# Kernel tuning notes

Measured on AMD Instinct MI355X. Metric: run time of the kernel, lower is better.

Reference implementation:

```python
import jax, jax.numpy as jnp
import numpy as np

FLOW_ITERS = 8
DUAL_ITERS = 8
DUAL_STEP = 0.1
DUAL_MOM = 0.9
GRAPH_LAYERS = 2
BIG = 1e9


def _sparsemax(z, mask):
    # sparsemax along last axis; masked entries already hold -BIG, zeroed by mask after.
    V = z.shape[-1]
    zs = jnp.sort(z, axis=-1)[..., ::-1]
    cum = jnp.cumsum(zs, axis=-1)
    k = jnp.arange(1, V + 1, dtype=z.dtype)
    support = zs * k > (cum - 1.0)
    k_sel = jnp.sum(support.astype(jnp.int32), axis=-1, keepdims=True)
    tau = (jnp.take_along_axis(cum, k_sel - 1, axis=-1) - 1.0) / k_sel.astype(z.dtype)
    return jnp.maximum(z - tau, 0.0) * mask


def _min_cost_flow(props, demands):
    # iterative proportional flow routing: push relu(inflow - demand) along predicted proportions
    def body(flow, _):
        inflow = jnp.sum(flow, axis=1)[..., None]      # [B,V,1] inflow to each node
        adjusted = jax.nn.relu(inflow - demands)       # excess to re-route
        return props * adjusted, None                  # row i scaled by its excess
    flow0 = jnp.zeros_like(props)
    flow, _ = jax.lax.scan(body, flow0, None, length=FLOW_ITERS)
    return flow


def _dual_flow(dual_diff, adj):
    # Nesterov-momentum projected gradient on cost(x)=x^2 minus linear dual term, x>=0 on edges
    def body(carry, _):
        flow, acc = carry
        look = flow - DUAL_MOM * acc
        grad = 2.0 * look - dual_diff                  # d/dx x^2 - dual_diff
        acc = DUAL_MOM * acc + DUAL_STEP * grad
        flow = adj * jax.nn.relu(flow - acc)
        return (flow, acc), None
    z = jnp.zeros_like(dual_diff)
    (flow, _), _ = jax.lax.scan(body, (z, z), None, length=DUAL_ITERS)
    return flow


def setup_inputs():
    key = jax.random.key(0)
    ks = jax.random.split(key, 32)
    B, V, F, E, D, K, H = 8, 1200, 8, 16, 64, 2, 4
    node_features = jax.random.normal(ks[0], (B, V, F), dtype=jnp.float32)
    node_embeddings = jax.random.normal(ks[1], (B, V, E), dtype=jnp.float32)
    d = jax.random.normal(ks[2], (B, V, 1), dtype=jnp.float32)
    demands = d - jnp.mean(d, axis=1, keepdims=True)   # balanced supply/demand per graph
    eye = jnp.eye(V, dtype=jnp.float32)
    adj = (jax.random.uniform(ks[3], (B, V, V)) < (16.0 / V)).astype(jnp.float32) * (1.0 - eye)
    hop2 = jnp.clip(adj @ adj, 0.0, 1.0) * (1.0 - eye)
    neighborhoods = jnp.stack([adj, hop2], axis=0)     # [K,B,V,V] k-hop neighborhoods

    def dense(k, fin, fout):
        return (jax.random.normal(k, (fin, fout), dtype=jnp.float32) / np.sqrt(fin)).astype(jnp.float32)

    return dict(
        node_features=node_features, node_embeddings=node_embeddings,
        demands=demands, adj=adj, neighborhoods=neighborhoods,
        enc_w0=dense(ks[4], E + F, D), enc_b0=jnp.zeros((D,), jnp.float32),
        enc_w1=dense(ks[5], D, D), enc_b1=jnp.zeros((D,), jnp.float32),
        agg_w=(jax.random.normal(ks[6], (K, D, D)) / np.sqrt(D)).astype(jnp.float32),
        agg_b=jnp.zeros((K, D), jnp.float32),
        att_w=(jax.random.normal(ks[7], (H, D, D)) / np.sqrt(D)).astype(jnp.float32),
        att_b=jnp.zeros((H, D), jnp.float32),
        att_v=(jax.random.normal(ks[8], (H, D)) / np.sqrt(D)).astype(jnp.float32),
        gru_wu=dense(ks[9], 2 * D, D), gru_bu=jnp.zeros((D,), jnp.float32),
        gru_wr=dense(ks[10], 2 * D, D), gru_br=jnp.zeros((D,), jnp.float32),
        gru_wc=dense(ks[11], 2 * D, D), gru_bc=jnp.zeros((D,), jnp.float32),
        dec_w0=dense(ks[12], D, D), dec_b0=jnp.zeros((D,), jnp.float32),
        dec_w1=dense(ks[13], D, 1), dec_b1=jnp.zeros((1,), jnp.float32),
        dual_w0=dense(ks[14], D, D), dual_b0=jnp.zeros((D,), jnp.float32),
        dual_w1=dense(ks[15], D, 1), dual_b1=jnp.zeros((1,), jnp.float32),
    )


def reference(node_features, node_embeddings, demands, adj, neighborhoods,
              enc_w0, enc_b0, enc_w1, enc_b1, agg_w, agg_b, att_w, att_b, att_v,
              gru_wu, gru_bu, gru_wr, gru_br, gru_wc, gru_bc,
              dec_w0, dec_b0, dec_w1, dec_b1, dual_w0, dual_b0, dual_w1, dual_b1):
    H = att_w.shape[0]
    # node encoder MLP (tanh hidden, tanh final since activate_final=True)
    x = jnp.concatenate([node_embeddings, node_features], axis=-1)
    enc = jnp.tanh(jnp.tanh(x @ enc_w0 + enc_b0) @ enc_w1 + enc_b1)            # [B,V,D]

    deg = jnp.sum(neighborhoods, axis=-1, keepdims=True)
    nb_norm = neighborhoods / jnp.maximum(deg, 1.0)                            # [K,B,V,V]

    for _ in range(GRAPH_LAYERS):
        # per-hop neighborhood aggregation
        msg = jnp.einsum('kbuv,bvd->kbud', nb_norm, enc)
        agg = jnp.tanh(jnp.einsum('kbud,kde->kbue', msg, agg_w) + agg_b[:, None, None, :])
        # multi-head attention over the K hop levels
        proj = jnp.tanh(jnp.einsum('kbvd,hde->hkbve', agg, att_w) + att_b[:, None, None, None, :])
        scores = jnp.einsum('hkbve,he->hkbv', proj, att_v)
        attn = jax.nn.softmax(scores, axis=1)                                  # softmax over hops
        nxt = jnp.einsum('hkbv,kbvd->bvd', attn, agg) / H                      # mean over heads
        # GRU state update
        xs = jnp.concatenate([nxt, enc], axis=-1)
        u = jax.nn.sigmoid(xs @ gru_wu + gru_bu)
        r = jax.nn.sigmoid(xs @ gru_wr + gru_br)
        c = jnp.tanh(jnp.concatenate([nxt, r * enc], axis=-1) @ gru_wc + gru_bc)
        enc = u * enc + (1.0 - u) * c

    # primal: edge weights -> sparsemax -> min-cost-flow
    pred = (enc @ dec_w0 + dec_b0) @ dec_w1 + dec_b1                           # [B,V,1]
    pred_weights = adj * jnp.transpose(pred, (0, 2, 1))                        # [B,V,V]
    weights = -BIG * (1.0 - adj) + pred_weights
    flow_props = _sparsemax(weights, adj)
    flow = _min_cost_flow(flow_props, demands)
    flow_cost = jnp.sum(flow * flow, axis=(1, 2))                              # square cost

    # dual: potentials -> dual-diff -> dual flow solver
    dual = (enc @ dual_w0 + dual_b0) @ dual_w1 + dual_b1                       # [B,V,1]
    dual_diff = adj * (dual - jnp.transpose(dual, (0, 2, 1)))
    dflow = _dual_flow(dual_diff, adj)
    dual_demand = jnp.sum(dual * demands, axis=(1, 2))
    dual_cost = jnp.sum(dflow * dflow - dual_diff * dflow, axis=(1, 2)) - dual_demand

    return flow_cost - dual_cost                                               # duality-gap loss, [B]
```

## Files before the change

kernel.cpp:

```cpp
#include <hip/hip_runtime.h>

#define BB 8
#define VV 1200
#define DD 64
#define KH 2
#define NH 4
#define CAP 64
#define NB2CAP 384
#define NROW (BB*VV)
#define NKROW (KH*BB*VV)

__device__ __forceinline__ float wredsum(float v) {
#pragma unroll
  for (int o = 32; o > 0; o >>= 1) v += __shfl_xor(v, o, 64);
  return v;
}
__device__ __forceinline__ float gredsum(float v) {
#pragma unroll
  for (int o = 8; o > 0; o >>= 1) v += __shfl_xor(v, o, 64);
  return v;
}

__device__ __forceinline__ float tanh_f(float x) {
  float e = __expf(2.0f * x);
  return 1.0f - 2.0f / (e + 1.0f);
}
__device__ __forceinline__ float sigmoid_f(float x) { return 1.0f / (1.0f + __expf(-x)); }

__device__ __forceinline__ unsigned pack_bf16x2(float a, float b) {
  unsigned ua = __float_as_uint(a), ub = __float_as_uint(b);
  ua = (ua + 0x7fffu + ((ua >> 16) & 1u)) >> 16;
  ub = (ub + 0x7fffu + ((ub >> 16) & 1u)) & 0xffff0000u;
  return ua | ub;
}
__device__ __forceinline__ float bf_lo(unsigned u) { return __uint_as_float(u << 16); }
__device__ __forceinline__ float bf_hi(unsigned u) { return __uint_as_float(u & 0xffff0000u); }

__device__ __forceinline__ size_t nb_base(int row) {
  return (row < NROW) ? (size_t)row * CAP
                      : (size_t)NROW * CAP + (size_t)(row - NROW) * NB2CAP;
}

#define CSRB (NKROW / 4)
#define ENCB (NROW / 8)
__global__ void __launch_bounds__(256) k_pre(
    const float* __restrict__ nb, int* __restrict__ nb_cols, int* __restrict__ nb_cnt,
    const float* __restrict__ emb, const float* __restrict__ feat,
    const float* __restrict__ w0, const float* __restrict__ b0,
    const float* __restrict__ w1, const float* __restrict__ b1,
    unsigned* __restrict__ enc0,
    int* __restrict__ col_cnt, float* __restrict__ out, int out_size) {
  __shared__ float xT[8][25];
  __shared__ float hT[8][65];
  int bid = blockIdx.x;
  int tid = threadIdx.x;
  if (bid < CSRB) {
    int w = tid >> 6, lane = tid & 63;
    int row = bid * 4 + w;
    const float4* nb4 = (const float4*)(nb + (size_t)row * VV);
    float4 v[5];
#pragma unroll
    for (int c = 0; c < 4; ++c) v[c] = nb4[c * 64 + lane];
    v[4].x = v[4].y = v[4].z = v[4].w = 0.0f;
    if (lane < 44) v[4] = nb4[256 + lane];
    unsigned long long ltmask = (lane == 0) ? 0ull : ((1ull << lane) - 1ull);
    size_t base = nb_base(row);
    int cap = (row < NROW) ? CAP : NB2CAP;
    int off_base = 0;
#pragma unroll
    for (int c = 0; c < 5; ++c) {
      int nz0 = (v[c].x != 0.0f), nz1 = (v[c].y != 0.0f);
      int nz2 = (v[c].z != 0.0f), nz3 = (v[c].w != 0.0f);
      unsigned long long m0 = __ballot(nz0 != 0);
      unsigned long long m1 = __ballot(nz1 != 0);
      unsigned long long m2 = __ballot(nz2 != 0);
      unsigned long long m3 = __ballot(nz3 != 0);
      int lanepref = __popcll(m0 & ltmask) + __popcll(m1 & ltmask)
                   + __popcll(m2 & ltmask) + __popcll(m3 & ltmask);
      int chunkcnt = __popcll(m0) + __popcll(m1) + __popcll(m2) + __popcll(m3);
      int off = off_base + lanepref;
      int vi = (c * 64 + lane) * 4;
      if (nz0 && off < cap) nb_cols[base + off] = vi;
      off += nz0;
      if (nz1 && off < cap) nb_cols[base + off] = vi + 1;
      off += nz1;
      if (nz2 && off < cap) nb_cols[base + off] = vi + 2;
      off += nz2;
      if (nz3 && off < cap) nb_cols[base + off] = vi + 3;
      off_base += chunkcnt;
    }
    if (lane == 0) nb_cnt[row] = (off_base > cap) ? cap : off_base;
  } else if (bid < CSRB + ENCB) {
    int tile0 = (bid - CSRB) * 8;
    if (tid < 128) { int i = tid >> 4, d = tid & 15; xT[i][d] = emb[(size_t)(tile0 + i) * 16 + d]; }
    else if (tid < 192) { int t = tid - 128; int i = t >> 3, d = t & 7; xT[i][16 + d] = feat[(size_t)(tile0 + i) * 8 + d]; }
    __syncthreads();
    int r = tid >> 5, cg = tid & 31;
    int c0 = cg * 2;
    {
      float a0 = b0[c0], a1 = b0[c0 + 1];
#pragma unroll
      for (int kk = 0; kk < 24; ++kk) {
        float x = xT[r][kk];
        float2 w2 = *(const float2*)(w0 + kk * DD + c0);
        a0 = fmaf(x, w2.x, a0); a1 = fmaf(x, w2.y, a1);
      }
      hT[r][c0] = tanh_f(a0); hT[r][c0 + 1] = tanh_f(a1);
    }
    __syncthreads();
    {
      float g0 = b1[c0], g1 = b1[c0 + 1];
#pragma unroll 16
      for (int kk = 0; kk < DD; ++kk) {
        float x = hT[r][kk];
        float2 w2 = *(const float2*)(w1 + kk * DD + c0);
        g0 = fmaf(x, w2.x, g0); g1 = fmaf(x, w2.y, g1);
      }
      enc0[(size_t)(tile0 + r) * 32 + cg] = pack_bf16x2(tanh_f(g0), tanh_f(g1));
    }
  } else {
    for (int i = tid; i < NROW; i += 256) col_cnt[i] = 0;
    if (tid < out_size) out[tid] = 0.0f;
  }
}

__global__ void __launch_bounds__(256) k_gather(
    const int* __restrict__ nb_cols, const int* __restrict__ nb_cnt,
    const unsigned* __restrict__ encIn, float* __restrict__ msg) {
  int w = threadIdx.x >> 6, lane = threadIdx.x & 63;
  int row = blockIdx.x * 4 + w;
  int k = (row >= NROW) ? 1 : 0;
  int bv = row - k * NROW;
  int b = bv / VV;
  const uint2* encU = (const uint2*)(encIn + (size_t)b * VV * 32);
  const int* cols = nb_cols + nb_base(row);
  int n = nb_cnt[row];
  int sub = lane >> 4, q = lane & 15;
  float ax = 0.0f, ay = 0.0f, az = 0.0f, aw = 0.0f;
  int j = 0;
  int cc0 = 0, cc1 = 0, cc2 = 0, cc3 = 0;
  if (j + 16 <= n) {
    cc0 = cols[j + sub]; cc1 = cols[j + 4 + sub];
    cc2 = cols[j + 8 + sub]; cc3 = cols[j + 12 + sub];
  }
  while (j + 16 <= n) {
    int nj = j + 16;
    int p0 = 0, p1 = 0, p2 = 0, p3 = 0;
    if (nj + 16 <= n) {
      p0 = cols[nj + sub]; p1 = cols[nj + 4 + sub];
      p2 = cols[nj + 8 + sub]; p3 = cols[nj + 12 + sub];
    }
    uint2 u0 = encU[(size_t)cc0 * 16 + q];
    uint2 u1 = encU[(size_t)cc1 * 16 + q];
    uint2 u2 = encU[(size_t)cc2 * 16 + q];
    uint2 u3 = encU[(size_t)cc3 * 16 + q];
    ax += (bf_lo(u0.x) + bf_lo(u1.x)) + (bf_lo(u2.x) + bf_lo(u3.x));
    ay += (bf_hi(u0.x) + bf_hi(u1.x)) + (bf_hi(u2.x) + bf_hi(u3.x));
    az += (bf_lo(u0.y) + bf_lo(u1.y)) + (bf_lo(u2.y) + bf_lo(u3.y));
    aw += (bf_hi(u0.y) + bf_hi(u1.y)) + (bf_hi(u2.y) + bf_hi(u3.y));
    cc0 = p0; cc1 = p1; cc2 = p2; cc3 = p3;
    j = nj;
  }
  for (; j < n; j += 4) {
    int idx = j + sub;
    if (idx < n) {
      uint2 u = encU[(size_t)cols[idx] * 16 + q];
      ax += bf_lo(u.x); ay += bf_hi(u.x); az += bf_lo(u.y); aw += bf_hi(u.y);
    }
  }
#pragma unroll
  for (int o = 16; o < 64; o <<= 1) {
    ax += __shfl_xor(ax, o, 64);
    ay += __shfl_xor(ay, o, 64);
    az += __shfl_xor(az, o, 64);
    aw += __shfl_xor(aw, o, 64);
  }
  if (lane < 16) {
    float inv = 1.0f / fmaxf((float)n, 1.0f);
    float4 r; r.x = ax * inv; r.y = ay * inv; r.z = az * inv; r.w = aw * inv;
    ((float4*)(msg + (size_t)row * DD))[q] = r;
  }
}

__global__ void __launch_bounds__(512) k_aggatt(
    const float* __restrict__ msg,
    const float* __restrict__ agg_w, const float* __restrict__ agg_b,
    const float* __restrict__ att_w, const float* __restrict__ att_b,
    const float* __restrict__ att_v,
    float* __restrict__ agg, float* __restrict__ scores) {
  __shared__ float M[64][65];
  __shared__ float G[64][65];
  int tid = threadIdx.x;
  int tile0 = blockIdx.x * 64;
  int k = (tile0 >= NROW) ? 1 : 0;
  int bv0 = tile0 - k * NROW;
  int rsub = tid >> 4, cg = tid & 15;
  int c0 = cg * 4;
  int r0 = rsub * 2;
#pragma unroll
  for (int rep = 0; rep < 2; ++rep) {
    int idx = rep * 512 + tid; int i = idx >> 4, d4 = idx & 15;
    float4 m4 = *(const float4*)(msg + (size_t)(tile0 + i) * DD + d4 * 4);
    M[i][d4 * 4] = m4.x; M[i][d4 * 4 + 1] = m4.y; M[i][d4 * 4 + 2] = m4.z; M[i][d4 * 4 + 3] = m4.w;
  }
  __syncthreads();
  const float* W = agg_w + (size_t)k * DD * DD;
  float acc[2][4];
#pragma unroll
  for (int i = 0; i < 2; ++i)
#pragma unroll
    for (int j = 0; j < 4; ++j) acc[i][j] = agg_b[k * DD + c0 + j];
#pragma unroll 4
  for (int kk = 0; kk < DD; ++kk) {
    float4 w4 = *(const float4*)(W + kk * DD + c0);
    float x0 = M[r0][kk], x1 = M[r0 + 1][kk];
    acc[0][0] = fmaf(x0, w4.x, acc[0][0]); acc[0][1] = fmaf(x0, w4.y, acc[0][1]);
    acc[0][2] = fmaf(x0, w4.z, acc[0][2]); acc[0][3] = fmaf(x0, w4.w, acc[0][3]);
    acc[1][0] = fmaf(x1, w4.x, acc[1][0]); acc[1][1] = fmaf(x1, w4.y, acc[1][1]);
    acc[1][2] = fmaf(x1, w4.z, acc[1][2]); acc[1][3] = fmaf(x1, w4.w, acc[1][3]);
  }
#pragma unroll
  for (int i = 0; i < 2; ++i) {
    float4 g4;
    g4.x = tanh_f(acc[i][0]); g4.y = tanh_f(acc[i][1]);
    g4.z = tanh_f(acc[i][2]); g4.w = tanh_f(acc[i][3]);
    G[r0 + i][c0] = g4.x; G[r0 + i][c0 + 1] = g4.y; G[r0 + i][c0 + 2] = g4.z; G[r0 + i][c0 + 3] = g4.w;
    *(float4*)(agg + (size_t)(tile0 + r0 + i) * DD + c0) = g4;
  }
  __syncthreads();
#pragma unroll
  for (int h = 0; h < NH; ++h) {
    const float* Wh = att_w + (size_t)h * DD * DD;
    float a2[2][4];
#pragma unroll
    for (int i = 0; i < 2; ++i)
#pragma unroll
      for (int j = 0; j < 4; ++j) a2[i][j] = att_b[h * DD + c0 + j];
#pragma unroll 4
    for (int kk = 0; kk < DD; ++kk) {
      float4 w4 = *(const float4*)(Wh + kk * DD + c0);
      float x0 = G[r0][kk], x1 = G[r0 + 1][kk];
      a2[0][0] = fmaf(x0, w4.x, a2[0][0]); a2[0][1] = fmaf(x0, w4.y, a2[0][1]);
      a2[0][2] = fmaf(x0, w4.z, a2[0][2]); a2[0][3] = fmaf(x0, w4.w, a2[0][3]);
      a2[1][0] = fmaf(x1, w4.x, a2[1][0]); a2[1][1] = fmaf(x1, w4.y, a2[1][1]);
      a2[1][2] = fmaf(x1, w4.z, a2[1][2]); a2[1][3] = fmaf(x1, w4.w, a2[1][3]);
    }
    float4 v4 = *(const float4*)(att_v + h * DD + c0);
#pragma unroll
    for (int i = 0; i < 2; ++i) {
      float p = tanh_f(a2[i][0]) * v4.x + tanh_f(a2[i][1]) * v4.y
              + tanh_f(a2[i][2]) * v4.z + tanh_f(a2[i][3]) * v4.w;
      p = gredsum(p);
      if (cg == 0) scores[(size_t)(h * KH + k) * NROW + bv0 + r0 + i] = p;
    }
  }
}

__global__ void __launch_bounds__(512) k_gru(
    const unsigned* __restrict__ encIn, const float* __restrict__ agg,
    const float* __restrict__ scores,
    const float* __restrict__ wu, const float* __restrict__ bu,
    const float* __restrict__ wr, const float* __restrict__ br,
    const float* __restrict__ wc, const float* __restrict__ bc,
    unsigned* __restrict__ encOut,
    int do_decode,
    const float* __restrict__ dw0, const float* __restrict__ db0,
    const float* __restrict__ dw1, const float* __restrict__ db1,
    const float* __restrict__ uw0, const float* __restrict__ ub0,
    const float* __restrict__ uw1, const float* __restrict__ ub1,
    float* __restrict__ pred, float* __restrict__ dualp) {
  __shared__ float X[64][129];
  __shared__ float EO[64][65];
  int tid = threadIdx.x;
  int tile0 = blockIdx.x * 64;
  int rsub = tid >> 4, cg = tid & 15;
  int c0 = cg * 4;
  int r0 = rsub * 2;
#pragma unroll
  for (int rep = 0; rep < 2; ++rep) {
    int idx = rep * 512 + tid; int i = idx >> 4, d4 = idx & 15;
    int row = tile0 + i;
    float W0 = 0.0f, W1 = 0.0f;
#pragma unroll
    for (int h = 0; h < NH; ++h) {
      float s0 = scores[(size_t)(h * KH + 0) * NROW + row];
      float s1 = scores[(size_t)(h * KH + 1) * NROW + row];
      float m = fmaxf(s0, s1);
      float e0 = __expf(s0 - m), e1 = __expf(s1 - m);
      float inv = 1.0f / (e0 + e1);
      W0 += e0 * inv; W1 += e1 * inv;
    }
    W0 *= 0.25f; W1 *= 0.25f;
    uint2 eu = ((const uint2*)encIn)[(size_t)row * 16 + d4];
    float4 a0 = *(const float4*)(agg + (size_t)row * DD + d4 * 4);
    float4 a1 = *(const float4*)(agg + (size_t)(NROW + row) * DD + d4 * 4);
    X[i][d4 * 4]     = W0 * a0.x + W1 * a1.x;
    X[i][d4 * 4 + 1] = W0 * a0.y + W1 * a1.y;
    X[i][d4 * 4 + 2] = W0 * a0.z + W1 * a1.z;
    X[i][d4 * 4 + 3] = W0 * a0.w + W1 * a1.w;
    X[i][64 + d4 * 4]     = bf_lo(eu.x);
    X[i][64 + d4 * 4 + 1] = bf_hi(eu.x);
    X[i][64 + d4 * 4 + 2] = bf_lo(eu.y);
    X[i][64 + d4 * 4 + 3] = bf_hi(eu.y);
  }
  __syncthreads();
  float au[2][4], ar[2][4];
#pragma unroll
  for (int i = 0; i < 2; ++i)
#pragma unroll
    for (int j = 0; j < 4; ++j) { au[i][j] = bu[c0 + j]; ar[i][j] = br[c0 + j]; }
#pragma unroll 4
  for (int kk = 0; kk < 2 * DD; ++kk) {
    float4 u4 = *(const float4*)(wu + kk * DD + c0);
    float4 r4 = *(const float4*)(wr + kk * DD + c0);
    float x0 = X[r0][kk], x1 = X[r0 + 1][kk];
    au[0][0] = fmaf(x0, u4.x, au[0][0]); au[0][1] = fmaf(x0, u4.y, au[0][1]);
    au[0][2] = fmaf(x0, u4.z, au[0][2]); au[0][3] = fmaf(x0, u4.w, au[0][3]);
    au[1][0] = fmaf(x1, u4.x, au[1][0]); au[1][1] = fmaf(x1, u4.y, au[1][1]);
    au[1][2] = fmaf(x1, u4.z, au[1][2]); au[1][3] = fmaf(x1, u4.w, au[1][3]);
    ar[0][0] = fmaf(x0, r4.x, ar[0][0]); ar[0][1] = fmaf(x0, r4.y, ar[0][1]);
    ar[0][2] = fmaf(x0, r4.z, ar[0][2]); ar[0][3] = fmaf(x0, r4.w, ar[0][3]);
    ar[1][0] = fmaf(x1, r4.x, ar[1][0]); ar[1][1] = fmaf(x1, r4.y, ar[1][1]);
    ar[1][2] = fmaf(x1, r4.z, ar[1][2]); ar[1][3] = fmaf(x1, r4.w, ar[1][3]);
  }
  float uu[2][4], encv[2][4];
#pragma unroll
  for (int i = 0; i < 2; ++i)
#pragma unroll
    for (int j = 0; j < 4; ++j) {
      uu[i][j] = sigmoid_f(au[i][j]);
      encv[i][j] = X[r0 + i][64 + c0 + j];
    }
  __syncthreads();
#pragma unroll
  for (int i = 0; i < 2; ++i)
#pragma unroll
    for (int j = 0; j < 4; ++j)
      X[r0 + i][64 + c0 + j] = encv[i][j] * sigmoid_f(ar[i][j]);
  __syncthreads();
  float ac[2][4];
#pragma unroll
  for (int i = 0; i < 2; ++i)
#pragma unroll
    for (int j = 0; j < 4; ++j) ac[i][j] = bc[c0 + j];
#pragma unroll 4
  for (int kk = 0; kk < 2 * DD; ++kk) {
    float4 c4 = *(const float4*)(wc + kk * DD + c0);
    float x0 = X[r0][kk], x1 = X[r0 + 1][kk];
    ac[0][0] = fmaf(x0, c4.x, ac[0][0]); ac[0][1] = fmaf(x0, c4.y, ac[0][1]);
    ac[0][2] = fmaf(x0, c4.z, ac[0][2]); ac[0][3] = fmaf(x0, c4.w, ac[0][3]);
    ac[1][0] = fmaf(x1, c4.x, ac[1][0]); ac[1][1] = fmaf(x1, c4.y, ac[1][1]);
    ac[1][2] = fmaf(x1, c4.z, ac[1][2]); ac[1][3] = fmaf(x1, c4.w, ac[1][3]);
  }
#pragma unroll
  for (int i = 0; i < 2; ++i) {
    float4 e4;
    e4.x = uu[i][0] * encv[i][0] + (1.0f - uu[i][0]) * tanh_f(ac[i][0]);
    e4.y = uu[i][1] * encv[i][1] + (1.0f - uu[i][1]) * tanh_f(ac[i][1]);
    e4.z = uu[i][2] * encv[i][2] + (1.0f - uu[i][2]) * tanh_f(ac[i][2]);
    e4.w = uu[i][3] * encv[i][3] + (1.0f - uu[i][3]) * tanh_f(ac[i][3]);
    uint2 pk; pk.x = pack_bf16x2(e4.x, e4.y); pk.y = pack_bf16x2(e4.z, e4.w);
    ((uint2*)encOut)[(size_t)(tile0 + r0 + i) * 16 + cg] = pk;
    EO[r0 + i][c0] = e4.x; EO[r0 + i][c0 + 1] = e4.y;
    EO[r0 + i][c0 + 2] = e4.z; EO[r0 + i][c0 + 3] = e4.w;
  }
  if (do_decode) {
    __syncthreads();
    float hd[2][4], hq[2][4];
#pragma unroll
    for (int i = 0; i < 2; ++i)
#pragma unroll
      for (int j = 0; j < 4; ++j) { hd[i][j] = db0[c0 + j]; hq[i][j] = ub0[c0 + j]; }
#pragma unroll 4
    for (int kk = 0; kk < DD; ++kk) {
      float4 d4 = *(const float4*)(dw0 + kk * DD + c0);
      float4 q4 = *(const float4*)(uw0 + kk * DD + c0);
      float x0 = EO[r0][kk], x1 = EO[r0 + 1][kk];
      hd[0][0] = fmaf(x0, d4.x, hd[0][0]); hd[0][1] = fmaf(x0, d4.y, hd[0][1]);
      hd[0][2] = fmaf(x0, d4.z, hd[0][2]); hd[0][3] = fmaf(x0, d4.w, hd[0][3]);
      hd[1][0] = fmaf(x1, d4.x, hd[1][0]); hd[1][1] = fmaf(x1, d4.y, hd[1][1]);
      hd[1][2] = fmaf(x1, d4.z, hd[1][2]); hd[1][3] = fmaf(x1, d4.w, hd[1][3]);
      hq[0][0] = fmaf(x0, q4.x, hq[0][0]); hq[0][1] = fmaf(x0, q4.y, hq[0][1]);
      hq[0][2] = fmaf(x0, q4.z, hq[0][2]); hq[0][3] = fmaf(x0, q4.w, hq[0][3]);
      hq[1][0] = fmaf(x1, q4.x, hq[1][0]); hq[1][1] = fmaf(x1, q4.y, hq[1][1]);
      hq[1][2] = fmaf(x1, q4.z, hq[1][2]); hq[1][3] = fmaf(x1, q4.w, hq[1][3]);
    }
    float4 dv = *(const float4*)(dw1 + c0);
    float4 qv = *(const float4*)(uw1 + c0);
#pragma unroll
    for (int i = 0; i < 2; ++i) {
      float p = hd[i][0] * dv.x + hd[i][1] * dv.y + hd[i][2] * dv.z + hd[i][3] * dv.w;
      float q = hq[i][0] * qv.x + hq[i][1] * qv.y + hq[i][2] * qv.z + hq[i][3] * qv.w;
      p = gredsum(p);
      q = gredsum(q);
      if (cg == 0) {
        pred[tile0 + r0 + i] = p + db1[0];
        dualp[tile0 + r0 + i] = q + ub1[0];
      }
    }
  }
}

__global__ void __launch_bounds__(256) k_primal_dual(
    const int* __restrict__ nb_cols, const int* __restrict__ nb_cnt,
    const float* __restrict__ pred, const float* __restrict__ dualp,
    const float* __restrict__ dem,
    float* __restrict__ rowsum,
    int* __restrict__ col_cnt, int* __restrict__ col_rows, float* __restrict__ col_vals,
    float* __restrict__ out) {
  __shared__ float bacc[BB];
  if (threadIdx.x < BB) bacc[threadIdx.x] = 0.0f;
  __syncthreads();
  int w = threadIdx.x >> 6, lane = threadIdx.x & 63;
  int row = blockIdx.x * 4 + w;
  int b = row / VV;
  int n = nb_cnt[row];
  int c = (lane < n) ? nb_cols[(size_t)row * CAP + lane] : 0;
  const float* predB = pred + (size_t)b * VV;
  const float* dualB = dualp + (size_t)b * VV;
  float z = (lane < n) ? predB[c] : -1e30f;
  float tau = 0.0f;
  if (n > 0) {
    bool in = (lane < n);
    for (int it = 0; it < 64; ++it) {
      float s = wredsum(in ? z : 0.0f);
      int cnt = (int)__popcll(__ballot(in));
      tau = (s - 1.0f) / (float)cnt;
      bool nin = (z > tau);
      if (__ballot(nin) == __ballot(in)) break;
      in = nin;
    }
  }
  float pv = (lane < n) ? fmaxf(z - tau, 0.0f) : 0.0f;
  float s2 = wredsum(pv * pv);
  if (lane == 0) rowsum[row] = s2;
  if (pv > 0.0f) {
    int g = b * VV + c;
    int j = atomicAdd(&col_cnt[g], 1);
    if (j < CAP) {
      col_rows[(size_t)g * CAP + j] = row - b * VV;
      col_vals[(size_t)g * CAP + j] = pv;
    }
  }
  float du = dualp[row];
  float es = 0.0f;
  if (lane < n) {
    float dd = du - dualB[c];
    float f = 0.0f, acm = 0.0f;
#pragma unroll
    for (int t = 0; t < 8; ++t) {
      float look = f - 0.9f * acm;
      float grad = 2.0f * look - dd;
      acm = 0.9f * acm + 0.1f * grad;
      f = fmaxf(f - acm, 0.0f);
    }
    es = f * f - dd * f;
  }
  float contrib = -es;
  if (lane == 0) contrib += du * dem[row];
  float ws_ = wredsum(contrib);
  if (lane == 0) atomicAdd(&bacc[b], ws_);
  __syncthreads();
  if (threadIdx.x < BB) {
    float t = bacc[threadIdx.x];
    if (t != 0.0f) atomicAdd(&out[threadIdx.x], t);
  }
}

__global__ void __launch_bounds__(1024) k_flow(
    const int* __restrict__ col_cnt, const int* __restrict__ col_rows,
    const float* __restrict__ col_vals, const float* __restrict__ dem,
    const float* __restrict__ rowsum, float* __restrict__ out) {
  __shared__ float aS[VV];
  __shared__ float red[16];
  int b = blockIdx.x;
  int tid = threadIdx.x;
  const float* demB = dem + (size_t)b * VV;
  for (int v = tid; v < VV; v += 1024) aS[v] = fmaxf(-demB[v], 0.0f);
  __syncthreads();
  for (int t = 0; t < 7; ++t) {
    float nv0 = 0.0f, nv1 = 0.0f;
    {
      int v = tid;
      if (v < VV) {
        int g = b * VV + v;
        int n = col_cnt[g]; if (n > CAP) n = CAP;
        const int* cr = col_rows + (size_t)g * CAP;
        const float* cv = col_vals + (size_t)g * CAP;
        float acc = 0.0f;
        for (int j = 0; j < n; ++j) acc += cv[j] * aS[cr[j]];
        nv0 = fmaxf(acc - demB[v], 0.0f);
      }
      v = tid + 1024;
      if (v < VV) {
        int g = b * VV + v;
        int n = col_cnt[g]; if (n > CAP) n = CAP;
        const int* cr = col_rows + (size_t)g * CAP;
        const float* cv = col_vals + (size_t)g * CAP;
        float acc = 0.0f;
        for (int j = 0; j < n; ++j) acc += cv[j] * aS[cr[j]];
        nv1 = fmaxf(acc - demB[v], 0.0f);
      }
    }
    __syncthreads();
    if (tid < VV) aS[tid] = nv0;
    if (tid + 1024 < VV) aS[tid + 1024] = nv1;
    __syncthreads();
  }
  float fc = 0.0f;
  for (int v = tid; v < VV; v += 1024) { float a = aS[v]; fc += a * a * rowsum[b * VV + v]; }
  fc = wredsum(fc);
  int wid = tid >> 6, lane = tid & 63;
  if (lane == 0) red[wid] = fc;
  __syncthreads();
  if (tid == 0) {
    float s = 0.0f;
#pragma unroll
    for (int i = 0; i < 16; ++i) s += red[i];
    atomicAdd(&out[b], s);
  }
}

extern "C" void kernel_launch(void* const* d_in, const int* in_sizes, int n_in,
                              void* d_out, int out_size, void* d_ws, size_t ws_size,
                              hipStream_t stream) {
  const float* feat   = (const float*)d_in[0];
  const float* emb    = (const float*)d_in[1];
  const float* dem    = (const float*)d_in[2];
  const float* nb     = (const float*)d_in[4];
  const float* enc_w0 = (const float*)d_in[5];
  const float* enc_b0 = (const float*)d_in[6];
  const float* enc_w1 = (const float*)d_in[7];
  const float* enc_b1 = (const float*)d_in[8];
  const float* agg_w  = (const float*)d_in[9];
  const float* agg_b  = (const float*)d_in[10];
  const float* att_w  = (const float*)d_in[11];
  const float* att_b  = (const float*)d_in[12];
  const float* att_v  = (const float*)d_in[13];
  const float* gru_wu = (const float*)d_in[14];
  const float* gru_bu = (const float*)d_in[15];
  const float* gru_wr = (const float*)d_in[16];
  const float* gru_br = (const float*)d_in[17];
  const float* gru_wc = (const float*)d_in[18];
  const float* gru_bc = (const float*)d_in[19];
  const float* dec_w0 = (const float*)d_in[20];
  const float* dec_b0 = (const float*)d_in[21];
  const float* dec_w1 = (const float*)d_in[22];
  const float* dec_b1 = (const float*)d_in[23];
  const float* dual_w0= (const float*)d_in[24];
  const float* dual_b0= (const float*)d_in[25];
  const float* dual_w1= (const float*)d_in[26];
  const float* dual_b1= (const float*)d_in[27];
  float* out = (float*)d_out;

  unsigned* enc0 = (unsigned*)d_ws;
  unsigned* enc1 = enc0 + (size_t)NROW * 32;
  float* msg      = (float*)(enc1 + (size_t)NROW * 32);
  float* aggbuf   = msg + (size_t)NKROW * DD;
  float* scores   = aggbuf + (size_t)NKROW * DD;
  float* pred     = scores + (size_t)NH * KH * NROW;
  float* dualp    = pred + NROW;
  float* rowsum   = dualp + NROW;
  float* col_vals = rowsum + NROW;
  int* col_cnt  = (int*)(col_vals + (size_t)NROW * CAP);
  int* nb_cnt   = col_cnt + NROW;
  int* col_rows = nb_cnt + NKROW;
  int* nb_cols  = col_rows + (size_t)NROW * CAP;

  (void)in_sizes; (void)n_in; (void)ws_size;

  k_pre<<<CSRB + ENCB + 1, 256, 0, stream>>>(
      nb, nb_cols, nb_cnt, emb, feat, enc_w0, enc_b0, enc_w1, enc_b1, enc0,
      col_cnt, out, out_size);

  const unsigned* encIn = enc0;
  unsigned* encOut = enc1;
  for (int l = 0; l < 2; ++l) {
    k_gather<<<NKROW / 4, 256, 0, stream>>>(nb_cols, nb_cnt, encIn, msg);
    k_aggatt<<<NKROW / 64, 512, 0, stream>>>(msg, agg_w, agg_b, att_w, att_b, att_v,
                                             aggbuf, scores);
    k_gru<<<NROW / 64, 512, 0, stream>>>(encIn, aggbuf, scores,
                                         gru_wu, gru_bu, gru_wr, gru_br, gru_wc, gru_bc,
                                         encOut,
                                         (l == 1) ? 1 : 0,
                                         dec_w0, dec_b0, dec_w1, dec_b1,
                                         dual_w0, dual_b0, dual_w1, dual_b1, pred, dualp);
    const unsigned* t = encIn; encIn = encOut; encOut = (unsigned*)t;
  }

  k_primal_dual<<<NROW / 4, 256, 0, stream>>>(nb_cols, nb_cnt, pred, dualp, dem,
                                              rowsum, col_cnt, col_rows, col_vals, out);
  k_flow<<<BB, 1024, 0, stream>>>(col_cnt, col_rows, col_vals, dem, rowsum, out);
}
```

Baseline: 546.7 us.

## Fuse neighbor gather into aggregation kernel and retile encoder precompute

The separate gather kernel that wrote mean-aggregated neighbor messages to global memory is folded into the aggregation/attention kernel. Each wave now computes eight rows' neighbor means directly into shared memory. This removes two kernel launches and a global round trip of the message buffer. The encoder MLP in the preprocessing kernel is also retiled to 64 rows per 512-thread block, and CSR extraction uses 8 rows per block. The cost is fewer blocks (300) running the gather with serial per-wave row loops, which may reduce memory-level parallelism for the irregular loads.

```diff
diff --git a/kernel.cpp b/kernel.cpp
--- a/kernel.cpp
+++ b/kernel.cpp
@@ -41,22 +41,78 @@
                       : (size_t)NROW * CAP + (size_t)(row - NROW) * NB2CAP;
 }
 
-#define CSRB (NKROW / 4)
-#define ENCB (NROW / 8)
-__global__ void __launch_bounds__(256) k_pre(
+#define ENC2B (NROW / 64)
+#define CSR2B (NKROW / 8)
+__global__ void __launch_bounds__(512) k_pre(
     const float* __restrict__ nb, int* __restrict__ nb_cols, int* __restrict__ nb_cnt,
     const float* __restrict__ emb, const float* __restrict__ feat,
     const float* __restrict__ w0, const float* __restrict__ b0,
     const float* __restrict__ w1, const float* __restrict__ b1,
     unsigned* __restrict__ enc0,
     int* __restrict__ col_cnt, float* __restrict__ out, int out_size) {
-  __shared__ float xT[8][25];
-  __shared__ float hT[8][65];
+  __shared__ float Xe[64][25];
+  __shared__ float Ht[64][65];
   int bid = blockIdx.x;
   int tid = threadIdx.x;
-  if (bid < CSRB) {
+  if (bid < ENC2B) {
+    int tile0 = bid * 64;
+    if (tid < 256) {
+      int i = tid >> 2, f = tid & 3;
+      float4 e4 = *(const float4*)(emb + (size_t)(tile0 + i) * 16 + f * 4);
+      Xe[i][f * 4] = e4.x; Xe[i][f * 4 + 1] = e4.y; Xe[i][f * 4 + 2] = e4.z; Xe[i][f * 4 + 3] = e4.w;
+    } else if (tid < 384) {
+      int t = tid - 256; int i = t >> 1, f = t & 1;
+      float4 f4 = *(const float4*)(feat + (size_t)(tile0 + i) * 8 + f * 4);
+      Xe[i][16 + f * 4] = f4.x; Xe[i][16 + f * 4 + 1] = f4.y;
+      Xe[i][16 + f * 4 + 2] = f4.z; Xe[i][16 + f * 4 + 3] = f4.w;
+    }
+    __syncthreads();
+    int rsub = tid >> 4, cg = tid & 15;
+    int c0 = cg * 4, r0 = rsub * 2;
+    float a[2][4];
+#pragma unroll
+    for (int i = 0; i < 2; ++i)
+#pragma unroll
+      for (int j = 0; j < 4; ++j) a[i][j] = b0[c0 + j];
+#pragma unroll
+    for (int kk = 0; kk < 24; ++kk) {
+      float4 w4 = *(const float4*)(w0 + kk * DD + c0);
+      float x0 = Xe[r0][kk], x1 = Xe[r0 + 1][kk];
+      a[0][0] = fmaf(x0, w4.x, a[0][0]); a[0][1] = fmaf(x0, w4.y, a[0][1]);
+      a[0][2] = fmaf(x0, w4.z, a[0][2]); a[0][3] = fmaf(x0, w4.w, a[0][3]);
+      a[1][0] = fmaf(x1, w4.x, a[1][0]); a[1][1] = fmaf(x1, w4.y, a[1][1]);
+      a[1][2] = fmaf(x1, w4.z, a[1][2]); a[1][3] = fmaf(x1, w4.w, a[1][3]);
+    }
+#pragma unroll
+    for (int i = 0; i < 2; ++i) {
+      Ht[r0 + i][c0] = tanh_f(a[i][0]); Ht[r0 + i][c0 + 1] = tanh_f(a[i][1]);
+      Ht[r0 + i][c0 + 2] = tanh_f(a[i][2]); Ht[r0 + i][c0 + 3] = tanh_f(a[i][3]);
+    }
+    __syncthreads();
+    float g[2][4];
+#pragma unroll
+    for (int i = 0; i < 2; ++i)
+#pragma unroll
+      for (int j = 0; j < 4; ++j) g[i][j] = b1[c0 + j];
+#pragma unroll 8
+    for (int kk = 0; kk < DD; ++kk) {
+      float4 w4 = *(const float4*)(w1 + kk * DD + c0);
+      float x0 = Ht[r0][kk], x1 = Ht[r0 + 1][kk];
+      g[0][0] = fmaf(x0, w4.x, g[0][0]); g[0][1] = fmaf(x0, w4.y, g[0][1]);
+      g[0][2] = fmaf(x0, w4.z, g[0][2]); g[0][3] = fmaf(x0, w4.w, g[0][3]);
+      g[1][0] = fmaf(x1, w4.x, g[1][0]); g[1][1] = fmaf(x1, w4.y, g[1][1]);
+      g[1][2] = fmaf(x1, w4.z, g[1][2]); g[1][3] = fmaf(x1, w4.w, g[1][3]);
+    }
+#pragma unroll
+    for (int i = 0; i < 2; ++i) {
+      uint2 pk;
+      pk.x = pack_bf16x2(tanh_f(g[i][0]), tanh_f(g[i][1]));
+      pk.y = pack_bf16x2(tanh_f(g[i][2]), tanh_f(g[i][3]));
+      ((uint2*)enc0)[(size_t)(tile0 + r0 + i) * 16 + cg] = pk;
+    }
+  } else if (bid < ENC2B + CSR2B) {
     int w = tid >> 6, lane = tid & 63;
-    int row = bid * 4 + w;
+    int row = (bid - ENC2B) * 8 + w;
     const float4* nb4 = (const float4*)(nb + (size_t)row * VV);
     float4 v[5];
 #pragma unroll
@@ -90,100 +146,15 @@
       off_base += chunkcnt;
     }
     if (lane == 0) nb_cnt[row] = (off_base > cap) ? cap : off_base;
-  } else if (bid < CSRB + ENCB) {
-    int tile0 = (bid - CSRB) * 8;
-    if (tid < 128) { int i = tid >> 4, d = tid & 15; xT[i][d] = emb[(size_t)(tile0 + i) * 16 + d]; }
-    else if (tid < 192) { int t = tid - 128; int i = t >> 3, d = t & 7; xT[i][16 + d] = feat[(size_t)(tile0 + i) * 8 + d]; }
-    __syncthreads();
-    int r = tid >> 5, cg = tid & 31;
-    int c0 = cg * 2;
-    {
-      float a0 = b0[c0], a1 = b0[c0 + 1];
-#pragma unroll
-      for (int kk = 0; kk < 24; ++kk) {
-        float x = xT[r][kk];
-        float2 w2 = *(const float2*)(w0 + kk * DD + c0);
-        a0 = fmaf(x, w2.x, a0); a1 = fmaf(x, w2.y, a1);
-      }
-      hT[r][c0] = tanh_f(a0); hT[r][c0 + 1] = tanh_f(a1);
-    }
-    __syncthreads();
-    {
-      float g0 = b1[c0], g1 = b1[c0 + 1];
-#pragma unroll 16
-      for (int kk = 0; kk < DD; ++kk) {
-        float x = hT[r][kk];
-        float2 w2 = *(const float2*)(w1 + kk * DD + c0);
-        g0 = fmaf(x, w2.x, g0); g1 = fmaf(x, w2.y, g1);
-      }
-      enc0[(size_t)(tile0 + r) * 32 + cg] = pack_bf16x2(tanh_f(g0), tanh_f(g1));
-    }
   } else {
-    for (int i = tid; i < NROW; i += 256) col_cnt[i] = 0;
+    for (int i = tid; i < NROW; i += 512) col_cnt[i] = 0;
     if (tid < out_size) out[tid] = 0.0f;
   }
 }
 
-__global__ void __launch_bounds__(256) k_gather(
+__global__ void __launch_bounds__(512) k_aggatt(
     const int* __restrict__ nb_cols, const int* __restrict__ nb_cnt,
-    const unsigned* __restrict__ encIn, float* __restrict__ msg) {
-  int w = threadIdx.x >> 6, lane = threadIdx.x & 63;
-  int row = blockIdx.x * 4 + w;
-  int k = (row >= NROW) ? 1 : 0;
-  int bv = row - k * NROW;
-  int b = bv / VV;
-  const uint2* encU = (const uint2*)(encIn + (size_t)b * VV * 32);
-  const int* cols = nb_cols + nb_base(row);
-  int n = nb_cnt[row];
-  int sub = lane >> 4, q = lane & 15;
-  float ax = 0.0f, ay = 0.0f, az = 0.0f, aw = 0.0f;
-  int j = 0;
-  int cc0 = 0, cc1 = 0, cc2 = 0, cc3 = 0;
-  if (j + 16 <= n) {
-    cc0 = cols[j + sub]; cc1 = cols[j + 4 + sub];
-    cc2 = cols[j + 8 + sub]; cc3 = cols[j + 12 + sub];
-  }
-  while (j + 16 <= n) {
-    int nj = j + 16;
-    int p0 = 0, p1 = 0, p2 = 0, p3 = 0;
-    if (nj + 16 <= n) {
-      p0 = cols[nj + sub]; p1 = cols[nj + 4 + sub];
-      p2 = cols[nj + 8 + sub]; p3 = cols[nj + 12 + sub];
-    }
-    uint2 u0 = encU[(size_t)cc0 * 16 + q];
-    uint2 u1 = encU[(size_t)cc1 * 16 + q];
-    uint2 u2 = encU[(size_t)cc2 * 16 + q];
-    uint2 u3 = encU[(size_t)cc3 * 16 + q];
-    ax += (bf_lo(u0.x) + bf_lo(u1.x)) + (bf_lo(u2.x) + bf_lo(u3.x));
-    ay += (bf_hi(u0.x) + bf_hi(u1.x)) + (bf_hi(u2.x) + bf_hi(u3.x));
-    az += (bf_lo(u0.y) + bf_lo(u1.y)) + (bf_lo(u2.y) + bf_lo(u3.y));
-    aw += (bf_hi(u0.y) + bf_hi(u1.y)) + (bf_hi(u2.y) + bf_hi(u3.y));
-    cc0 = p0; cc1 = p1; cc2 = p2; cc3 = p3;
-    j = nj;
-  }
-  for (; j < n; j += 4) {
-    int idx = j + sub;
-    if (idx < n) {
-      uint2 u = encU[(size_t)cols[idx] * 16 + q];
-      ax += bf_lo(u.x); ay += bf_hi(u.x); az += bf_lo(u.y); aw += bf_hi(u.y);
-    }
-  }
-#pragma unroll
-  for (int o = 16; o < 64; o <<= 1) {
-    ax += __shfl_xor(ax, o, 64);
-    ay += __shfl_xor(ay, o, 64);
-    az += __shfl_xor(az, o, 64);
-    aw += __shfl_xor(aw, o, 64);
-  }
-  if (lane < 16) {
-    float inv = 1.0f / fmaxf((float)n, 1.0f);
-    float4 r; r.x = ax * inv; r.y = ay * inv; r.z = az * inv; r.w = aw * inv;
-    ((float4*)(msg + (size_t)row * DD))[q] = r;
-  }
-}
-
-__global__ void __launch_bounds__(512) k_aggatt(
-    const float* __restrict__ msg,
+    const unsigned* __restrict__ encIn,
     const float* __restrict__ agg_w, const float* __restrict__ agg_b,
     const float* __restrict__ att_w, const float* __restrict__ att_b,
     const float* __restrict__ att_v,
@@ -194,16 +165,65 @@
   int tile0 = blockIdx.x * 64;
   int k = (tile0 >= NROW) ? 1 : 0;
   int bv0 = tile0 - k * NROW;
+  int wid = tid >> 6, lane = tid & 63;
+  int sub = lane >> 4, q = lane & 15;
+  for (int ii = 0; ii < 8; ++ii) {
+    int i = wid * 8 + ii;
+    int row = tile0 + i;
+    int bv = row - k * NROW;
+    int b = bv / VV;
+    const uint2* encU = (const uint2*)(encIn + (size_t)b * VV * 32);
+    const int* cols = nb_cols + nb_base(row);
+    int n = nb_cnt[row];
+    float ax = 0.0f, ay = 0.0f, az = 0.0f, aw = 0.0f;
+    int j = 0;
+    int cc0 = 0, cc1 = 0, cc2 = 0, cc3 = 0;
+    if (j + 16 <= n) {
+      cc0 = cols[j + sub]; cc1 = cols[j + 4 + sub];
+      cc2 = cols[j + 8 + sub]; cc3 = cols[j + 12 + sub];
+    }
+    while (j + 16 <= n) {
+      int nj = j + 16;
+      int p0 = 0, p1 = 0, p2 = 0, p3 = 0;
+      if (nj + 16 <= n) {
+        p0 = cols[nj + sub]; p1 = cols[nj + 4 + sub];
+        p2 = cols[nj + 8 + sub]; p3 = cols[nj + 12 + sub];
+      }
+      uint2 u0 = encU[(size_t)cc0 * 16 + q];
+      uint2 u1 = encU[(size_t)cc1 * 16 + q];
+      uint2 u2 = encU[(size_t)cc2 * 16 + q];
+      uint2 u3 = encU[(size_t)cc3 * 16 + q];
+      ax += (bf_lo(u0.x) + bf_lo(u1.x)) + (bf_lo(u2.x) + bf_lo(u3.x));
+      ay += (bf_hi(u0.x) + bf_hi(u1.x)) + (bf_hi(u2.x) + bf_hi(u3.x));
+      az += (bf_lo(u0.y) + bf_lo(u1.y)) + (bf_lo(u2.y) + bf_lo(u3.y));
+      aw += (bf_hi(u0.y) + bf_hi(u1.y)) + (bf_hi(u2.y) + bf_hi(u3.y));
+      cc0 = p0; cc1 = p1; cc2 = p2; cc3 = p3;
+      j = nj;
+    }
+    for (; j < n; j += 4) {
+      int idx = j + sub;
+      if (idx < n) {
+        uint2 u = encU[(size_t)cols[idx] * 16 + q];
+        ax += bf_lo(u.x); ay += bf_hi(u.x); az += bf_lo(u.y); aw += bf_hi(u.y);
+      }
+    }
+#pragma unroll
+    for (int o = 16; o < 64; o <<= 1) {
+      ax += __shfl_xor(ax, o, 64);
+      ay += __shfl_xor(ay, o, 64);
+      az += __shfl_xor(az, o, 64);
+      aw += __shfl_xor(aw, o, 64);
+    }
+    if (lane < 16) {
+      float inv = 1.0f / fmaxf((float)n, 1.0f);
+      M[i][q * 4] = ax * inv; M[i][q * 4 + 1] = ay * inv;
+      M[i][q * 4 + 2] = az * inv; M[i][q * 4 + 3] = aw * inv;
+    }
+  }
+  __syncthreads();
   int rsub = tid >> 4, cg = tid & 15;
   int c0 = cg * 4;
   int r0 = rsub * 2;
-#pragma unroll
-  for (int rep = 0; rep < 2; ++rep) {
-    int idx = rep * 512 + tid; int i = idx >> 4, d4 = idx & 15;
-    float4 m4 = *(const float4*)(msg + (size_t)(tile0 + i) * DD + d4 * 4);
-    M[i][d4 * 4] = m4.x; M[i][d4 * 4 + 1] = m4.y; M[i][d4 * 4 + 2] = m4.z; M[i][d4 * 4 + 3] = m4.w;
-  }
-  __syncthreads();
   const float* W = agg_w + (size_t)k * DD * DD;
   float acc[2][4];
 #pragma unroll
@@ -569,15 +589,15 @@
 
   (void)in_sizes; (void)n_in; (void)ws_size;
 
-  k_pre<<<CSRB + ENCB + 1, 256, 0, stream>>>(
+  k_pre<<<ENC2B + CSR2B + 1, 512, 0, stream>>>(
       nb, nb_cols, nb_cnt, emb, feat, enc_w0, enc_b0, enc_w1, enc_b1, enc0,
       col_cnt, out, out_size);
 
   const unsigned* encIn = enc0;
   unsigned* encOut = enc1;
   for (int l = 0; l < 2; ++l) {
-    k_gather<<<NKROW / 4, 256, 0, stream>>>(nb_cols, nb_cnt, encIn, msg);
-    k_aggatt<<<NKROW / 64, 512, 0, stream>>>(msg, agg_w, agg_b, att_w, att_b, att_v,
+    k_aggatt<<<NKROW / 64, 512, 0, stream>>>(nb_cols, nb_cnt, encIn,
+                                             agg_w, agg_b, att_w, att_b, att_v,
                                              aggbuf, scores);
     k_gru<<<NROW / 64, 512, 0, stream>>>(encIn, aggbuf, scores,
                                          gru_wu, gru_bu, gru_wr, gru_br, gru_wc, gru_bc,
```

Result: slower. 598.6 us (+9.5%).
